# Performance work log

Hardware: AMD Instinct MI355X
Metric: run time of the kernel (lower is better)

Reference implementation:

```python
import jax, jax.numpy as jnp
import numpy as np

B, C, H, W = 16, 15, 256, 256

def setup_inputs() -> dict:
    key = jax.random.key(0)
    k1, k2, k3 = jax.random.split(key, 3)
    output = jax.random.normal(k1, (B, C, H, W), dtype=jnp.float32)
    label0 = jax.random.normal(k2, (B, C, H, W), dtype=jnp.float32)
    label1 = jax.random.uniform(k3, (B, C, H, W), dtype=jnp.float32)
    return {"output": output, "label0": label0, "label1": label1}

def reference(output, label0, label1):
    # Fused masked-L1 reduction over the whole tensor (replaces per-(b,c) loop)
    loss = jnp.sum(jnp.abs(output - label0) * label1)
    nonzero_num = jnp.sum(label0 != 0)  # total count of nonzero target entries
    # if nonzero_num == 0: loss -> 0, denom -> 1
    safe_denom = jnp.where(nonzero_num == 0, 1, nonzero_num).astype(loss.dtype)
    loss = jnp.where(nonzero_num == 0, jnp.zeros_like(loss), loss)
    return loss / safe_denom
```

## Files before the change

kernel.cpp:

```cpp
#include <hip/hip_runtime.h>
#include <hip/hip_bf16.h>


#define REDUCE_THREADS 256
#define EPT 8

struct Partial {
    float s;
    unsigned int c;
};

__global__ __launch_bounds__(REDUCE_THREADS)
void depth_loss_stage1(const float4* __restrict__ out,
                       const float4* __restrict__ l0,
                       const float4* __restrict__ l1,
                       Partial* __restrict__ partials,
                       int n4) {
    const int base = blockIdx.x * (REDUCE_THREADS * EPT) + threadIdx.x;

    float4 o[EPT], a[EPT], w[EPT];
    #pragma unroll
    for (int k = 0; k < EPT; ++k) {
        int i = base + k * REDUCE_THREADS;
        bool ok = (i < n4);
        int j = ok ? i : 0;
        o[k] = out[j];
        a[k] = l0[j];
        w[k] = l1[j];
        if (!ok) {
            a[k] = make_float4(0.f, 0.f, 0.f, 0.f);
            o[k] = make_float4(0.f, 0.f, 0.f, 0.f);
            w[k] = make_float4(0.f, 0.f, 0.f, 0.f);
        }
    }

    float sum = 0.0f;
    unsigned int cnt = 0;
    #pragma unroll
    for (int k = 0; k < EPT; ++k) {
        sum += fabsf(o[k].x - a[k].x) * w[k].x;
        sum += fabsf(o[k].y - a[k].y) * w[k].y;
        sum += fabsf(o[k].z - a[k].z) * w[k].z;
        sum += fabsf(o[k].w - a[k].w) * w[k].w;
        cnt += (a[k].x != 0.0f) + (a[k].y != 0.0f) +
               (a[k].z != 0.0f) + (a[k].w != 0.0f);
    }

    #pragma unroll
    for (int off = 32; off > 0; off >>= 1) {
        sum += __shfl_down(sum, off, 64);
        cnt += __shfl_down(cnt, off, 64);
    }

    __shared__ float        sv[REDUCE_THREADS / 64];
    __shared__ unsigned int sc[REDUCE_THREADS / 64];
    int lane = threadIdx.x & 63;
    int wid  = threadIdx.x >> 6;
    if (lane == 0) { sv[wid] = sum; sc[wid] = cnt; }
    __syncthreads();

    if (threadIdx.x == 0) {
        float bs = 0.0f;
        unsigned int bc = 0;
        #pragma unroll
        for (int i = 0; i < REDUCE_THREADS / 64; ++i) { bs += sv[i]; bc += sc[i]; }
        Partial p; p.s = bs; p.c = bc;
        partials[blockIdx.x] = p;
    }
}

__global__ __launch_bounds__(REDUCE_THREADS)
void depth_loss_stage2(const Partial* __restrict__ partials,
                       int nblocks,
                       float* __restrict__ out) {
    double sum = 0.0;
    unsigned int cnt = 0;
    for (int i = threadIdx.x; i < nblocks; i += REDUCE_THREADS) {
        Partial p = partials[i];
        sum += (double)p.s;
        cnt += p.c;
    }

    #pragma unroll
    for (int off = 32; off > 0; off >>= 1) {
        sum += __shfl_down(sum, off, 64);
        cnt += __shfl_down(cnt, off, 64);
    }

    __shared__ double       sv[REDUCE_THREADS / 64];
    __shared__ unsigned int sc[REDUCE_THREADS / 64];
    int lane = threadIdx.x & 63;
    int wid  = threadIdx.x >> 6;
    if (lane == 0) { sv[wid] = sum; sc[wid] = cnt; }
    __syncthreads();

    if (threadIdx.x == 0) {
        double bs = 0.0;
        unsigned int bc = 0;
        #pragma unroll
        for (int i = 0; i < REDUCE_THREADS / 64; ++i) { bs += sv[i]; bc += sc[i]; }
        out[0] = (bc == 0) ? 0.0f : (float)(bs / (double)bc);
    }
}

extern "C" void kernel_launch(void* const* d_in, const int* in_sizes, int n_in,
                              void* d_out, int out_size, void* d_ws, size_t ws_size,
                              hipStream_t stream) {
    const float* output = (const float*)d_in[0];
    const float* label0 = (const float*)d_in[1];
    const float* label1 = (const float*)d_in[2];
    int n = in_sizes[0];
    int n4 = n >> 2;

    int per_block = REDUCE_THREADS * EPT;
    int blocks = (n4 + per_block - 1) / per_block;

    Partial* partials = (Partial*)d_ws;

    depth_loss_stage1<<<blocks, REDUCE_THREADS, 0, stream>>>(
        (const float4*)output, (const float4*)label0, (const float4*)label1,
        partials, n4);

    depth_loss_stage2<<<1, REDUCE_THREADS, 0, stream>>>(
        partials, blocks, (float*)d_out);
}
```

Before: 187.7 us.

## Switch stage-1 reduction to fixed-size grid-stride loop with 2x unrolled exact path

Replaces the one-shot grid sized to the data (8 float4 per thread) with a fixed 1920-block grid-stride loop, and adds a specialised path that unrolls by two when the element count divides evenly. This shrinks the number of partials and block launch overhead and keeps loads in flight across iterations. The risk is lower memory-level parallelism per thread than the prior 8-deep batch of loads, and a fixed grid size tuned to the device.

```diff
diff --git a/kernel.cpp b/kernel.cpp
--- a/kernel.cpp
+++ b/kernel.cpp
@@ -1,49 +1,55 @@
 #include <hip/hip_runtime.h>
-#include <hip/hip_bf16.h>
 
 
 #define REDUCE_THREADS 256
-#define EPT 8
+#define S1_BLOCKS 1920
 
 struct Partial {
     float s;
     unsigned int c;
 };
 
+__device__ __forceinline__ void accum4(const float4& o, const float4& a,
+                                       const float4& w, float& sum,
+                                       unsigned int& cnt) {
+    sum += fabsf(o.x - a.x) * w.x;
+    sum += fabsf(o.y - a.y) * w.y;
+    sum += fabsf(o.z - a.z) * w.z;
+    sum += fabsf(o.w - a.w) * w.w;
+    cnt += (a.x != 0.0f) + (a.y != 0.0f) + (a.z != 0.0f) + (a.w != 0.0f);
+}
+
+template <bool EXACT2>
 __global__ __launch_bounds__(REDUCE_THREADS)
 void depth_loss_stage1(const float4* __restrict__ out,
                        const float4* __restrict__ l0,
                        const float4* __restrict__ l1,
                        Partial* __restrict__ partials,
                        int n4) {
-    const int base = blockIdx.x * (REDUCE_THREADS * EPT) + threadIdx.x;
-
-    float4 o[EPT], a[EPT], w[EPT];
-    #pragma unroll
-    for (int k = 0; k < EPT; ++k) {
-        int i = base + k * REDUCE_THREADS;
-        bool ok = (i < n4);
-        int j = ok ? i : 0;
-        o[k] = out[j];
-        a[k] = l0[j];
-        w[k] = l1[j];
-        if (!ok) {
-            a[k] = make_float4(0.f, 0.f, 0.f, 0.f);
-            o[k] = make_float4(0.f, 0.f, 0.f, 0.f);
-            w[k] = make_float4(0.f, 0.f, 0.f, 0.f);
-        }
-    }
+    const int stride = gridDim.x * REDUCE_THREADS;
+    int i = blockIdx.x * REDUCE_THREADS + threadIdx.x;
 
     float sum = 0.0f;
     unsigned int cnt = 0;
-    #pragma unroll
-    for (int k = 0; k < EPT; ++k) {
-        sum += fabsf(o[k].x - a[k].x) * w[k].x;
-        sum += fabsf(o[k].y - a[k].y) * w[k].y;
-        sum += fabsf(o[k].z - a[k].z) * w[k].z;
-        sum += fabsf(o[k].w - a[k].w) * w[k].w;
-        cnt += (a[k].x != 0.0f) + (a[k].y != 0.0f) +
-               (a[k].z != 0.0f) + (a[k].w != 0.0f);
+
+    if constexpr (EXACT2) {
+        for (; i < n4; i += 2 * stride) {
+            float4 o0 = out[i];
+            float4 a0 = l0[i];
+            float4 w0 = l1[i];
+            float4 o1 = out[i + stride];
+            float4 a1 = l0[i + stride];
+            float4 w1 = l1[i + stride];
+            accum4(o0, a0, w0, sum, cnt);
+            accum4(o1, a1, w1, sum, cnt);
+        }
+    } else {
+        for (; i < n4; i += stride) {
+            float4 o0 = out[i];
+            float4 a0 = l0[i];
+            float4 w0 = l1[i];
+            accum4(o0, a0, w0, sum, cnt);
+        }
     }
 
     #pragma unroll
@@ -63,7 +69,7 @@
         float bs = 0.0f;
         unsigned int bc = 0;
         #pragma unroll
-        for (int i = 0; i < REDUCE_THREADS / 64; ++i) { bs += sv[i]; bc += sc[i]; }
+        for (int i2 = 0; i2 < REDUCE_THREADS / 64; ++i2) { bs += sv[i2]; bc += sc[i2]; }
         Partial p; p.s = bs; p.c = bc;
         partials[blockIdx.x] = p;
     }
@@ -112,15 +118,18 @@
     int n = in_sizes[0];
     int n4 = n >> 2;
 
-    int per_block = REDUCE_THREADS * EPT;
-    int blocks = (n4 + per_block - 1) / per_block;
-
     Partial* partials = (Partial*)d_ws;
 
-    depth_loss_stage1<<<blocks, REDUCE_THREADS, 0, stream>>>(
-        (const float4*)output, (const float4*)label0, (const float4*)label1,
-        partials, n4);
+    if ((n4 % (S1_BLOCKS * REDUCE_THREADS * 2)) == 0) {
+        depth_loss_stage1<true><<<S1_BLOCKS, REDUCE_THREADS, 0, stream>>>(
+            (const float4*)output, (const float4*)label0, (const float4*)label1,
+            partials, n4);
+    } else {
+        depth_loss_stage1<false><<<S1_BLOCKS, REDUCE_THREADS, 0, stream>>>(
+            (const float4*)output, (const float4*)label0, (const float4*)label1,
+            partials, n4);
+    }
 
     depth_loss_stage2<<<1, REDUCE_THREADS, 0, stream>>>(
-        partials, blocks, (float*)d_out);
+        partials, S1_BLOCKS, (float*)d_out);
 }
```

New measurement: 190.9 us. Within noise of the previous version (+1.7%).
